# Optimization experiments

Measured on AMD Instinct MI355X. Metric: run time of the kernel, lower is better.

## Reference

```python
import jax, jax.numpy as jnp
import numpy as np
import math

D_EMBED = 1024
N_HEADS = 16
HEAD_DIM = D_EMBED // N_HEADS
ROPE_BASE = 10000.0


def apply_rope(x):
    # x: [B, S, H, D] ; torchtune-style interleaved RoPE
    B, S, H, D = x.shape
    half = D // 2
    inv_freq = 1.0 / (ROPE_BASE ** (jnp.arange(0, D, 2, dtype=jnp.float32) / D))  # [half]
    angles = jnp.arange(S, dtype=jnp.float32)[:, None] * inv_freq[None, :]        # [S, half]
    cos = jnp.cos(angles)[None, :, None, :].astype(x.dtype)  # [1,S,1,half]
    sin = jnp.sin(angles)[None, :, None, :].astype(x.dtype)
    x1 = x[..., 0::2]
    x2 = x[..., 1::2]
    o1 = x1 * cos - x2 * sin
    o2 = x1 * sin + x2 * cos
    return jnp.stack([o1, o2], axis=-1).reshape(B, S, H, D)


def setup_inputs() -> dict:
    key = jax.random.key(0)
    ks = jax.random.split(key, 7)
    B, S = 4, 2048
    d_tri = D_EMBED
    q = jax.random.normal(ks[0], (B, S, 2 * d_tri), dtype=jnp.float32)
    k = jax.random.normal(ks[1], (B, S, 2 * d_tri), dtype=jnp.float32)
    v = jax.random.normal(ks[2], (B, S, d_tri), dtype=jnp.float32)
    s_in = 1.0 / math.sqrt(2 * d_tri)
    s_tri = 1.0 / math.sqrt(d_tri)
    W_q = jax.random.normal(ks[3], (D_EMBED, 2 * d_tri), dtype=jnp.float32) * s_in
    W_k = jax.random.normal(ks[4], (D_EMBED, 2 * d_tri), dtype=jnp.float32) * s_in
    W_v = jax.random.normal(ks[5], (d_tri, d_tri), dtype=jnp.float32) * s_tri
    W_o = jax.random.normal(ks[6], (d_tri, d_tri), dtype=jnp.float32) * s_tri
    return {"q": q, "k": k, "v": v, "W_q": W_q, "W_k": W_k, "W_v": W_v, "W_o": W_o}


def reference(q, k, v, W_q, W_k, W_v, W_o):
    B, S, _ = q.shape
    H, Dh = N_HEADS, HEAD_DIM
    scale = 1.0 / math.sqrt(D_EMBED)

    qp = (q @ W_q.T).reshape(B, S, H, Dh)
    kp = (k @ W_k.T).reshape(B, S, H, Dh)
    vp = (v @ W_v.T).reshape(B, S, H, Dh)

    qp = apply_rope(qp)
    kp = apply_rope(kp)

    # [B,H,S,S]
    scores = jnp.einsum('bqhd,bkhd->bhqk', qp, kp) * scale
    causal = jnp.tril(jnp.ones((S, S), dtype=bool))
    scores = jnp.where(causal[None, None], scores, -jnp.inf)
    probs = jax.nn.softmax(scores, axis=-1)
    # dropout layers are identity in eval mode
    out = jnp.einsum('bhqk,bkhd->bqhd', probs, vp).reshape(B, S, D_EMBED)
    return out @ W_o.T
```

## Files before the change

kernel.cpp:

```cpp
#include <hip/hip_runtime.h>
#include <math.h>

#define S_LEN 2048
#define DEMB  1024
#define DH    64

typedef short bf16x8 __attribute__((ext_vector_type(8)));
typedef short bf16x4 __attribute__((ext_vector_type(4)));
typedef float floatx4 __attribute__((ext_vector_type(4)));

__device__ __forceinline__ short f2bf(float f) {
    unsigned u = __builtin_bit_cast(unsigned, f);
    u += 0x7FFFu + ((u >> 16) & 1u);
    return (short)(u >> 16);
}

__global__ void rope_table_k(float2* __restrict__ tab) {
    int idx = blockIdx.x * 256 + threadIdx.x;
    int s = idx >> 5, i = idx & 31;
    double ang = (double)s * pow(10000.0, -(double)i / 32.0);
    tab[idx] = make_float2((float)cos(ang), (float)sin(ang));
}

struct CvtArgs { const float* src[7]; short* dst[7]; int n[7]; };
__global__ __launch_bounds__(256) void cvt_k(CvtArgs a) {
    int seg = blockIdx.y;
    int idx = (blockIdx.x * 256 + threadIdx.x) * 8;
    if (idx >= a.n[seg]) return;
    const float4* s = (const float4*)(a.src[seg] + idx);
    float4 v0 = s[0], v1 = s[1];
    bf16x8 r;
    r[0] = f2bf(v0.x); r[1] = f2bf(v0.y); r[2] = f2bf(v0.z); r[3] = f2bf(v0.w);
    r[4] = f2bf(v1.x); r[5] = f2bf(v1.y); r[6] = f2bf(v1.z); r[7] = f2bf(v1.w);
    *(bf16x8*)(a.dst[seg] + idx) = r;
}

__device__ __forceinline__ void gld16(const void* g, void* l) {
    __builtin_amdgcn_global_load_lds(
        (const __attribute__((address_space(1))) void*)g,
        (__attribute__((address_space(3))) void*)l, 16, 0, 0);
}

template<int EPI>
__device__ __forceinline__ void gemm_b16_body(
    const short* __restrict__ A, const short* __restrict__ B,
    void* __restrict__ Cout, const float2* __restrict__ rope_tab,
    int M, int N, int K, short* smem)
{
    short* sA = smem;
    short* sB = smem + 128 * 32;

    const int tid  = threadIdx.x;
    const int lane = tid & 63;
    const int wv   = tid >> 6;
    const int wm   = wv >> 1, wn = wv & 1;
    const int lr   = lane & 15, quad = lane >> 4;
    const int m0   = blockIdx.y * 128, n0 = blockIdx.x * 128;

    const int rowS = tid >> 2;
    const int kkS  = (tid & 3) * 8;
    const short* gA0 = A + (size_t)(m0 + rowS) * K + kkS;
    const short* gA1 = gA0 + (size_t)64 * K;
    const short* gB0 = B + (size_t)(n0 + rowS) * K + kkS;
    const short* gB1 = gB0 + (size_t)64 * K;
    short* lA0 = sA + wv * 512;
    short* lA1 = sA + 2048 + wv * 512;
    short* lB0 = sB + wv * 512;
    short* lB1 = sB + 2048 + wv * 512;

    floatx4 acc[4][4] = {};

    for (int k0 = 0; k0 < K; k0 += 32) {
        gld16(gA0 + k0, lA0);
        gld16(gA1 + k0, lA1);
        gld16(gB0 + k0, lB0);
        gld16(gB1 + k0, lB1);
        __syncthreads();
        bf16x8 af[4], bfr[4];
        #pragma unroll
        for (int t = 0; t < 4; t++)
            af[t] = *reinterpret_cast<const bf16x8*>(&sA[(wm * 64 + t * 16 + lr) * 32 + quad * 8]);
        #pragma unroll
        for (int t = 0; t < 4; t++)
            bfr[t] = *reinterpret_cast<const bf16x8*>(&sB[(wn * 64 + t * 16 + lr) * 32 + quad * 8]);
        #pragma unroll
        for (int mt = 0; mt < 4; mt++)
            #pragma unroll
            for (int nt = 0; nt < 4; nt++)
                acc[mt][nt] = __builtin_amdgcn_mfma_f32_16x16x32_bf16(af[mt], bfr[nt], acc[mt][nt], 0, 0, 0);
        __syncthreads();
    }

    if constexpr (EPI == 0) {
        short* C = (short*)Cout;
        #pragma unroll
        for (int nt = 0; nt < 4; nt++) {
            int n_g = n0 + wn * 64 + nt * 16 + lr;
            int ii  = (n_g & 63) >> 1;
            bool evenc = (n_g & 1) == 0;
            #pragma unroll
            for (int mt = 0; mt < 4; mt++) {
                #pragma unroll
                for (int r = 0; r < 4; r++) {
                    int m_g = m0 + wm * 64 + mt * 16 + quad * 4 + r;
                    float2 cs = rope_tab[(m_g & (S_LEN - 1)) * 32 + ii];
                    float v  = acc[mt][nt][r];
                    float vn = __shfl_xor(v, 1);
                    float o = evenc ? (v * cs.x - vn * cs.y) : (v * cs.x + vn * cs.y);
                    C[(size_t)m_g * N + n_g] = f2bf(o);
                }
            }
        }
    } else if constexpr (EPI == 2) {
        float* C = (float*)Cout;
        #pragma unroll
        for (int mt = 0; mt < 4; mt++)
            #pragma unroll
            for (int r = 0; r < 4; r++) {
                size_t rowoff = (size_t)(m0 + wm * 64 + mt * 16 + quad * 4 + r) * N;
                #pragma unroll
                for (int nt = 0; nt < 4; nt++)
                    C[rowoff + n0 + wn * 64 + nt * 16 + lr] = acc[mt][nt][r];
            }
    } else {
        short* sT = smem;
        __syncthreads();
        #pragma unroll
        for (int nt = 0; nt < 4; nt++) {
            int nl = wn * 64 + nt * 16 + lr;
            #pragma unroll
            for (int mt = 0; mt < 4; mt++)
                #pragma unroll
                for (int r = 0; r < 4; r++)
                    sT[nl * 136 + wm * 64 + mt * 16 + quad * 4 + r] = f2bf(acc[mt][nt][r]);
        }
        __syncthreads();
        short* C = (short*)Cout;
        int bb = m0 >> 11;
        int s_base = m0 & (S_LEN - 1);
        #pragma unroll
        for (int i = 0; i < 8; i++) {
            int col = (tid >> 4) + i * 16;
            int mc  = (tid & 15) * 8;
            bf16x8 v = *reinterpret_cast<const bf16x8*>(&sT[col * 136 + mc]);
            size_t row = (size_t)bb * DEMB + (n0 + col);
            *reinterpret_cast<bf16x8*>(&C[row * S_LEN + s_base + mc]) = v;
        }
    }
}

template<int EPI>
__global__ __launch_bounds__(256) void gemm_b16(
    const short* __restrict__ A, const short* __restrict__ B,
    void* __restrict__ Cout, const float2* __restrict__ rope_tab,
    int M, int N, int K)
{
    __shared__ __align__(16) short smem[(EPI == 1) ? (128 * 136) : (128 * 64)];
    gemm_b16_body<EPI>(A, B, Cout, rope_tab, M, N, K, smem);
}

__global__ __launch_bounds__(256) void gemm_qk(
    const short* __restrict__ Aq, const short* __restrict__ Bq, void* __restrict__ Cq,
    const short* __restrict__ Ak, const short* __restrict__ Bk, void* __restrict__ Ck,
    const float2* __restrict__ rope_tab, int M, int N, int K)
{
    __shared__ __align__(16) short smem[128 * 64];
    if (blockIdx.z == 0)
        gemm_b16_body<0>(Aq, Bq, Cq, rope_tab, M, N, K, smem);
    else
        gemm_b16_body<0>(Ak, Bk, Ck, rope_tab, M, N, K, smem);
}

__global__ __launch_bounds__(256, 3) void flash_k(
    const short* __restrict__ qp, const short* __restrict__ kp,
    const short* __restrict__ vpT, short* __restrict__ attn)
{
    __shared__ __align__(16) short sKV[2][2][4096];
    __shared__ __align__(16) short sPb[4][2048];

    const int tid = threadIdx.x;
    const int w = tid >> 6, lane = tid & 63, lr = lane & 15, quad = lane >> 4;
    const int qt = 15 - (blockIdx.x >> 6);
    const int bh = blockIdx.x & 63;
    const int b = bh >> 4, h = bh & 15;
    const int R = qt * 128 + w * 32;
    const size_t qbase = (size_t)(b * S_LEN) * DEMB + h * DH;

    const short* kbase = kp + qbase;
    const short* vbase = vpT + ((size_t)(b * DEMB) + h * DH) * S_LEN;

    const int srow = tid >> 3;
    const int sp   = tid & 7;
    const int cs   = (sp ^ (srow & 7)) * 8;
    short* dK0 = &sKV[0][0][w * 512];  short* dV0 = &sKV[0][1][w * 512];
    short* dK1 = &sKV[1][0][w * 512];  short* dV1 = &sKV[1][1][w * 512];

    bf16x8 qf[2][2];
    #pragma unroll
    for (int mt = 0; mt < 2; mt++)
        #pragma unroll
        for (int ks = 0; ks < 2; ks++)
            qf[mt][ks] = *reinterpret_cast<const bf16x8*>(
                &qp[qbase + (size_t)(R + mt * 16 + lr) * DEMB + ks * 32 + quad * 8]);

    floatx4 oacc[2][4] = {};
    float lsum[2][4] = {};
    const float CEXP = 0.045084220081510574f;
    short* pw = sPb[w];

    const int ktend = 2 * qt + 1;

    auto stage = [&](int kt, int buf) {
        const short* kg = kbase + (size_t)kt * 64 * DEMB;
        const short* vg = vbase + kt * 64;
        short* dK = buf ? dK1 : dK0;
        short* dV = buf ? dV1 : dV0;
        gld16(kg + (size_t)srow * DEMB + cs,        dK);
        gld16(kg + (size_t)(srow + 32) * DEMB + cs, dK + 2048);
        gld16(vg + (size_t)srow * S_LEN + cs,       dV);
        gld16(vg + (size_t)(srow + 32) * S_LEN + cs, dV + 2048);
    };

    stage(0, 0);
    __syncthreads();

    for (int kt = 0; kt <= ktend; kt++) {
        const int cur = kt & 1;
        if (kt < ktend) stage(kt + 1, cur ^ 1);

        if (R + 31 >= kt * 64) {
            const short* sK = sKV[cur][0];
            const short* sV = sKV[cur][1];

            bf16x8 kf[4][2], vf[4][2];
            #pragma unroll
            for (int nt = 0; nt < 4; nt++)
                #pragma unroll
                for (int ks = 0; ks < 2; ks++) {
                    int ph = (ks * 4 + quad) ^ (lr & 7);
                    kf[nt][ks] = *reinterpret_cast<const bf16x8*>(&sK[(nt * 16 + lr) * 64 + ph * 8]);
                    vf[nt][ks] = *reinterpret_cast<const bf16x8*>(&sV[(nt * 16 + lr) * 64 + ph * 8]);
                }

            floatx4 st[2][4];
            #pragma unroll
            for (int nt = 0; nt < 4; nt++)
                #pragma unroll
                for (int mt = 0; mt < 2; mt++) {
                    floatx4 z = {};
                    z = __builtin_amdgcn_mfma_f32_16x16x32_bf16(qf[mt][0], kf[nt][0], z, 0, 0, 0);
                    st[mt][nt] = __builtin_amdgcn_mfma_f32_16x16x32_bf16(qf[mt][1], kf[nt][1], z, 0, 0, 0);
                }

            const bool need_mask = (kt * 64 + 63 > R);
            #pragma unroll
            for (int mt = 0; mt < 2; mt++)
                #pragma unroll
                for (int nt = 0; nt < 4; nt++)
                    #pragma unroll
                    for (int r = 0; r < 4; r++) {
                        float t = fminf(st[mt][nt][r] * CEXP, 80.f);
                        float p = __builtin_amdgcn_exp2f(t);
                        if (need_mask) {
                            int col = kt * 64 + nt * 16 + lr;
                            int row = R + mt * 16 + quad * 4 + r;
                            p = (col > row) ? 0.f : p;
                        }
                        st[mt][nt][r] = p;
                        lsum[mt][r] += p;
                    }

            #pragma unroll
            for (int mt = 0; mt < 2; mt++)
                #pragma unroll
                for (int nt = 0; nt < 4; nt++)
                    #pragma unroll
                    for (int r = 0; r < 4; r++) {
                        int rw = mt * 16 + quad * 4 + r;
                        int chunk = (nt * 2 + (lr >> 3)) ^ (rw & 7);
                        pw[rw * 64 + chunk * 8 + (lr & 7)] = f2bf(st[mt][nt][r]);
                    }

            bf16x8 pf[2][2];
            #pragma unroll
            for (int mt = 0; mt < 2; mt++)
                #pragma unroll
                for (int ks = 0; ks < 2; ks++) {
                    int rr = mt * 16 + lr;
                    int c  = (ks * 4 + quad) ^ (rr & 7);
                    pf[mt][ks] = *reinterpret_cast<const bf16x8*>(&pw[rr * 64 + c * 8]);
                }

            #pragma unroll
            for (int d = 0; d < 4; d++)
                #pragma unroll
                for (int mt = 0; mt < 2; mt++) {
                    oacc[mt][d] = __builtin_amdgcn_mfma_f32_16x16x32_bf16(pf[mt][0], vf[d][0], oacc[mt][d], 0, 0, 0);
                    oacc[mt][d] = __builtin_amdgcn_mfma_f32_16x16x32_bf16(pf[mt][1], vf[d][1], oacc[mt][d], 0, 0, 0);
                }
        }
        __syncthreads();
    }

    #pragma unroll
    for (int mt = 0; mt < 2; mt++)
        #pragma unroll
        for (int r = 0; r < 4; r++) {
            float l = lsum[mt][r];
            l += __shfl_xor(l, 1);
            l += __shfl_xor(l, 2);
            l += __shfl_xor(l, 4);
            l += __shfl_xor(l, 8);
            float inv = 1.f / l;
            size_t rowoff = qbase + (size_t)(R + mt * 16 + quad * 4 + r) * DEMB;
            #pragma unroll
            for (int d = 0; d < 4; d++)
                attn[rowoff + d * 16 + lr] = f2bf(oacc[mt][d][r] * inv);
        }
}

__device__ __forceinline__ bf16x4 load4(const float* p) {
    const float4 v = *reinterpret_cast<const float4*>(p);
    bf16x4 r; r[0] = f2bf(v.x); r[1] = f2bf(v.y); r[2] = f2bf(v.z); r[3] = f2bf(v.w);
    return r;
}
__device__ __forceinline__ bf16x4 load4(const short* p) {
    return *reinterpret_cast<const bf16x4*>(p);
}

template<typename TA, int EPI>
__global__ __launch_bounds__(256) void gemm_nt(
    const TA* __restrict__ A, const float* __restrict__ B,
    void* __restrict__ Cout, const float2* __restrict__ rope_tab,
    int M, int N, int K)
{
    __shared__ __align__(16) short smem[(EPI == 1) ? (128 * 136) : (2 * 128 * 40)];
    short* sA = smem;
    short* sB = smem + 128 * 40;

    const int tid  = threadIdx.x;
    const int lane = tid & 63;
    const int wv   = tid >> 6;
    const int wm   = wv >> 1, wn = wv & 1;
    const int lr   = lane & 15, quad = lane >> 4;
    const int m0   = blockIdx.y * 128, n0 = blockIdx.x * 128;

    floatx4 acc[4][4] = {};

    for (int k0 = 0; k0 < K; k0 += 32) {
        #pragma unroll
        for (int i = 0; i < 4; i++) {
            int c = tid + i * 256;
            int row = c >> 3, kc = (c & 7) << 2;
            bf16x4 v = load4(&A[(size_t)(m0 + row) * K + k0 + kc]);
            *reinterpret_cast<bf16x4*>(&sA[row * 40 + kc]) = v;
        }
        #pragma unroll
        for (int i = 0; i < 4; i++) {
            int c = tid + i * 256;
            int row = c >> 3, kc = (c & 7) << 2;
            bf16x4 v = load4(&B[(size_t)(n0 + row) * K + k0 + kc]);
            *reinterpret_cast<bf16x4*>(&sB[row * 40 + kc]) = v;
        }
        __syncthreads();
        bf16x8 af[4], bfr[4];
        #pragma unroll
        for (int t = 0; t < 4; t++)
            af[t] = *reinterpret_cast<const bf16x8*>(&sA[(wm * 64 + t * 16 + lr) * 40 + quad * 8]);
        #pragma unroll
        for (int t = 0; t < 4; t++)
            bfr[t] = *reinterpret_cast<const bf16x8*>(&sB[(wn * 64 + t * 16 + lr) * 40 + quad * 8]);
        #pragma unroll
        for (int mt = 0; mt < 4; mt++)
            #pragma unroll
            for (int nt = 0; nt < 4; nt++)
                acc[mt][nt] = __builtin_amdgcn_mfma_f32_16x16x32_bf16(af[mt], bfr[nt], acc[mt][nt], 0, 0, 0);
        __syncthreads();
    }

    if constexpr (EPI == 0) {
        short* C = (short*)Cout;
        #pragma unroll
        for (int nt = 0; nt < 4; nt++) {
            int n_g = n0 + wn * 64 + nt * 16 + lr;
            int ii  = (n_g & 63) >> 1;
            bool evenc = (n_g & 1) == 0;
            #pragma unroll
            for (int mt = 0; mt < 4; mt++) {
                #pragma unroll
                for (int r = 0; r < 4; r++) {
                    int m_g = m0 + wm * 64 + mt * 16 + quad * 4 + r;
                    float2 cs = rope_tab[(m_g & (S_LEN - 1)) * 32 + ii];
                    float v  = acc[mt][nt][r];
                    float vn = __shfl_xor(v, 1);
                    float o = evenc ? (v * cs.x - vn * cs.y) : (v * cs.x + vn * cs.y);
                    C[(size_t)m_g * N + n_g] = f2bf(o);
                }
            }
        }
    } else if constexpr (EPI == 2) {
        float* C = (float*)Cout;
        #pragma unroll
        for (int mt = 0; mt < 4; mt++)
            #pragma unroll
            for (int r = 0; r < 4; r++) {
                size_t rowoff = (size_t)(m0 + wm * 64 + mt * 16 + quad * 4 + r) * N;
                #pragma unroll
                for (int nt = 0; nt < 4; nt++)
                    C[rowoff + n0 + wn * 64 + nt * 16 + lr] = acc[mt][nt][r];
            }
    } else {
        short* sT = smem;
        __syncthreads();
        #pragma unroll
        for (int nt = 0; nt < 4; nt++) {
            int nl = wn * 64 + nt * 16 + lr;
            #pragma unroll
            for (int mt = 0; mt < 4; mt++)
                #pragma unroll
                for (int r = 0; r < 4; r++)
                    sT[nl * 136 + wm * 64 + mt * 16 + quad * 4 + r] = f2bf(acc[mt][nt][r]);
        }
        __syncthreads();
        short* C = (short*)Cout;
        int bb = m0 >> 11;
        int s_base = m0 & (S_LEN - 1);
        #pragma unroll
        for (int i = 0; i < 8; i++) {
            int col = (tid >> 4) + i * 16;
            int mc  = (tid & 15) * 8;
            bf16x8 v = *reinterpret_cast<const bf16x8*>(&sT[col * 136 + mc]);
            size_t row = (size_t)bb * DEMB + (n0 + col);
            *reinterpret_cast<bf16x8*>(&C[row * S_LEN + s_base + mc]) = v;
        }
    }
}

extern "C" void kernel_launch(void* const* d_in, const int* in_sizes, int n_in,
                              void* d_out, int out_size, void* d_ws, size_t ws_size,
                              hipStream_t stream) {
    const float* q  = (const float*)d_in[0];
    const float* k  = (const float*)d_in[1];
    const float* v  = (const float*)d_in[2];
    const float* Wq = (const float*)d_in[3];
    const float* Wk = (const float*)d_in[4];
    const float* Wv = (const float*)d_in[5];
    const float* Wo = (const float*)d_in[6];
    float* out = (float*)d_out;

    char* ws = (char*)d_ws;
    const size_t MB = 1024 * 1024;
    short*  qp   = (short*)(ws);
    short*  kp   = (short*)(ws + 16 * MB);
    short*  vpT  = (short*)(ws + 32 * MB);
    short*  attn = (short*)(ws + 48 * MB);
    float2* tab  = (float2*)(ws + 64 * MB);

    rope_table_k<<<256, 256, 0, stream>>>(tab);

    dim3 g2(8, 64);
    if (ws_size >= 157 * MB) {
        short* qb  = (short*)(ws + 65 * MB);
        short* kb  = (short*)(ws + 97 * MB);
        short* vb  = (short*)(ws + 129 * MB);
        short* wqb = (short*)(ws + 145 * MB);
        short* wkb = (short*)(ws + 149 * MB);
        short* wvb = (short*)(ws + 153 * MB);
        short* wob = (short*)(ws + 155 * MB);

        CvtArgs ca;
        ca.src[0] = q;  ca.dst[0] = qb;  ca.n[0] = 16777216;
        ca.src[1] = k;  ca.dst[1] = kb;  ca.n[1] = 16777216;
        ca.src[2] = v;  ca.dst[2] = vb;  ca.n[2] = 8388608;
        ca.src[3] = Wq; ca.dst[3] = wqb; ca.n[3] = 2097152;
        ca.src[4] = Wk; ca.dst[4] = wkb; ca.n[4] = 2097152;
        ca.src[5] = Wv; ca.dst[5] = wvb; ca.n[5] = 1048576;
        ca.src[6] = Wo; ca.dst[6] = wob; ca.n[6] = 1048576;
        cvt_k<<<dim3(8192, 7), 256, 0, stream>>>(ca);

        gemm_qk<<<dim3(8, 64, 2), 256, 0, stream>>>(qb, wqb, qp, kb, wkb, kp, tab, 8192, 1024, 2048);
        gemm_b16<1><<<g2, 256, 0, stream>>>(vb, wvb, vpT, nullptr, 8192, 1024, 1024);
        flash_k<<<1024, 256, 0, stream>>>(qp, kp, vpT, attn);
        gemm_b16<2><<<g2, 256, 0, stream>>>(attn, wob, out, nullptr, 8192, 1024, 1024);
    } else {
        gemm_nt<float, 0><<<g2, 256, 0, stream>>>(q, Wq, qp,  tab,     8192, 1024, 2048);
        gemm_nt<float, 0><<<g2, 256, 0, stream>>>(k, Wk, kp,  tab,     8192, 1024, 2048);
        gemm_nt<float, 1><<<g2, 256, 0, stream>>>(v, Wv, vpT, nullptr, 8192, 1024, 1024);
        flash_k<<<1024, 256, 0, stream>>>(qp, kp, vpT, attn);
        gemm_nt<short, 2><<<g2, 256, 0, stream>>>(attn, Wo, out, nullptr, 8192, 1024, 1024);
    }
}
```

Before: 442.6 us.

## Widen GEMM K-tile to 64 with swizzled LDS and merge QKV projections

```diff
diff --git a/kernel.cpp b/kernel.cpp
--- a/kernel.cpp
+++ b/kernel.cpp
@@ -42,13 +42,13 @@
 }
 
 template<int EPI>
-__device__ __forceinline__ void gemm_b16_body(
+__device__ __forceinline__ void gemm_body(
     const short* __restrict__ A, const short* __restrict__ B,
     void* __restrict__ Cout, const float2* __restrict__ rope_tab,
-    int M, int N, int K, short* smem)
+    int K, short* smem)
 {
     short* sA = smem;
-    short* sB = smem + 128 * 32;
+    short* sB = smem + 8192;
 
     const int tid  = threadIdx.x;
     const int lane = tid & 63;
@@ -56,60 +56,77 @@
     const int wm   = wv >> 1, wn = wv & 1;
     const int lr   = lane & 15, quad = lane >> 4;
     const int m0   = blockIdx.y * 128, n0 = blockIdx.x * 128;
-
-    const int rowS = tid >> 2;
-    const int kkS  = (tid & 3) * 8;
-    const short* gA0 = A + (size_t)(m0 + rowS) * K + kkS;
-    const short* gA1 = gA0 + (size_t)64 * K;
-    const short* gB0 = B + (size_t)(n0 + rowS) * K + kkS;
-    const short* gB1 = gB0 + (size_t)64 * K;
-    short* lA0 = sA + wv * 512;
-    short* lA1 = sA + 2048 + wv * 512;
-    short* lB0 = sB + wv * 512;
-    short* lB1 = sB + 2048 + wv * 512;
+    const int N    = 1024;
+
+    const short* gA[4]; const short* gB[4];
+    #pragma unroll
+    for (int j = 0; j < 4; j++) {
+        int c = j * 256 + tid;
+        int row = c >> 3, sp = c & 7;
+        int cs = (sp ^ (row & 7)) * 8;
+        gA[j] = A + (size_t)(m0 + row) * K + cs;
+        gB[j] = B + (size_t)(n0 + row) * K + cs;
+    }
 
     floatx4 acc[4][4] = {};
 
-    for (int k0 = 0; k0 < K; k0 += 32) {
-        gld16(gA0 + k0, lA0);
-        gld16(gA1 + k0, lA1);
-        gld16(gB0 + k0, lB0);
-        gld16(gB1 + k0, lB1);
-        __syncthreads();
-        bf16x8 af[4], bfr[4];
+    for (int k0 = 0; k0 < K; k0 += 64) {
+        #pragma unroll
+        for (int j = 0; j < 4; j++) {
+            gld16(gA[j] + k0, sA + j * 2048 + wv * 512);
+            gld16(gB[j] + k0, sB + j * 2048 + wv * 512);
+        }
+        __syncthreads();
+        bf16x8 af[4][2], bfr[4][2];
         #pragma unroll
         for (int t = 0; t < 4; t++)
-            af[t] = *reinterpret_cast<const bf16x8*>(&sA[(wm * 64 + t * 16 + lr) * 32 + quad * 8]);
-        #pragma unroll
-        for (int t = 0; t < 4; t++)
-            bfr[t] = *reinterpret_cast<const bf16x8*>(&sB[(wn * 64 + t * 16 + lr) * 32 + quad * 8]);
-        #pragma unroll
-        for (int mt = 0; mt < 4; mt++)
-            #pragma unroll
-            for (int nt = 0; nt < 4; nt++)
-                acc[mt][nt] = __builtin_amdgcn_mfma_f32_16x16x32_bf16(af[mt], bfr[nt], acc[mt][nt], 0, 0, 0);
+            #pragma unroll
+            for (int ks = 0; ks < 2; ks++) {
+                int ph = (ks * 4 + quad) ^ (lr & 7);
+                af[t][ks]  = *reinterpret_cast<const bf16x8*>(&sA[(wm * 64 + t * 16 + lr) * 64 + ph * 8]);
+                bfr[t][ks] = *reinterpret_cast<const bf16x8*>(&sB[(wn * 64 + t * 16 + lr) * 64 + ph * 8]);
+            }
+        #pragma unroll
+        for (int ks = 0; ks < 2; ks++)
+            #pragma unroll
+            for (int mt = 0; mt < 4; mt++)
+                #pragma unroll
+                for (int nt = 0; nt < 4; nt++)
+                    acc[mt][nt] = __builtin_amdgcn_mfma_f32_16x16x32_bf16(af[mt][ks], bfr[nt][ks], acc[mt][nt], 0, 0, 0);
         __syncthreads();
     }
 
     if constexpr (EPI == 0) {
-        short* C = (short*)Cout;
+        unsigned* sTi = (unsigned*)smem;
         #pragma unroll
         for (int nt = 0; nt < 4; nt++) {
-            int n_g = n0 + wn * 64 + nt * 16 + lr;
-            int ii  = (n_g & 63) >> 1;
-            bool evenc = (n_g & 1) == 0;
-            #pragma unroll
-            for (int mt = 0; mt < 4; mt++) {
+            int n_l = wn * 64 + nt * 16 + lr;
+            int ii  = ((n0 + n_l) & 63) >> 1;
+            #pragma unroll
+            for (int mt = 0; mt < 4; mt++)
                 #pragma unroll
                 for (int r = 0; r < 4; r++) {
-                    int m_g = m0 + wm * 64 + mt * 16 + quad * 4 + r;
-                    float2 cs = rope_tab[(m_g & (S_LEN - 1)) * 32 + ii];
+                    int row_l = wm * 64 + mt * 16 + quad * 4 + r;
+                    float2 cs = rope_tab[((m0 + row_l) & (S_LEN - 1)) * 32 + ii];
                     float v  = acc[mt][nt][r];
                     float vn = __shfl_xor(v, 1);
-                    float o = evenc ? (v * cs.x - vn * cs.y) : (v * cs.x + vn * cs.y);
-                    C[(size_t)m_g * N + n_g] = f2bf(o);
+                    float o0 = v * cs.x - vn * cs.y;
+                    float o1 = vn * cs.x + v * cs.y;
+                    if (!(lr & 1)) {
+                        unsigned pk = (unsigned)(unsigned short)f2bf(o0) |
+                                      ((unsigned)(unsigned short)f2bf(o1) << 16);
+                        sTi[row_l * 68 + (n_l >> 1)] = pk;
+                    }
                 }
-            }
+        }
+        __syncthreads();
+        short* C = (short*)Cout;
+        #pragma unroll
+        for (int j = 0; j < 8; j++) {
+            int c = j * 256 + tid;
+            int row = c >> 4, col = (c & 15) * 8;
+            bf16x8 val = *reinterpret_cast<const bf16x8*>(&smem[row * 136 + col]);
+            *reinterpret_cast<bf16x8*>(&C[(size_t)(m0 + row) * N + n0 + col]) = val;
         }
     } else if constexpr (EPI == 2) {
         float* C = (float*)Cout;
@@ -124,7 +141,6 @@
             }
     } else {
         short* sT = smem;
-        __syncthreads();
         #pragma unroll
         for (int nt = 0; nt < 4; nt++) {
             int nl = wn * 64 + nt * 16 + lr;
@@ -149,26 +165,26 @@
     }
 }
 
-template<int EPI>
-__global__ __launch_bounds__(256) void gemm_b16(
-    const short* __restrict__ A, const short* __restrict__ B,
-    void* __restrict__ Cout, const float2* __restrict__ rope_tab,
-    int M, int N, int K)
-{
-    __shared__ __align__(16) short smem[(EPI == 1) ? (128 * 136) : (128 * 64)];
-    gemm_b16_body<EPI>(A, B, Cout, rope_tab, M, N, K, smem);
-}
-
-__global__ __launch_bounds__(256) void gemm_qk(
+__global__ __launch_bounds__(256, 3) void gemm_proj(
     const short* __restrict__ Aq, const short* __restrict__ Bq, void* __restrict__ Cq,
     const short* __restrict__ Ak, const short* __restrict__ Bk, void* __restrict__ Ck,
-    const float2* __restrict__ rope_tab, int M, int N, int K)
+    const short* __restrict__ Av, const short* __restrict__ Bv, void* __restrict__ Cv,
+    const float2* __restrict__ rope_tab)
 {
-    __shared__ __align__(16) short smem[128 * 64];
+    __shared__ __align__(16) short smem[17408];
     if (blockIdx.z == 0)
-        gemm_b16_body<0>(Aq, Bq, Cq, rope_tab, M, N, K, smem);
+        gemm_body<0>(Aq, Bq, Cq, rope_tab, 2048, smem);
+    else if (blockIdx.z == 1)
+        gemm_body<0>(Ak, Bk, Ck, rope_tab, 2048, smem);
     else
-        gemm_b16_body<0>(Ak, Bk, Ck, rope_tab, M, N, K, smem);
+        gemm_body<1>(Av, Bv, Cv, nullptr, 1024, smem);
+}
+
+__global__ __launch_bounds__(256, 3) void gemm_out(
+    const short* __restrict__ A, const short* __restrict__ B, void* __restrict__ Cout)
+{
+    __shared__ __align__(16) short smem[17408];
+    gemm_body<2>(A, B, Cout, nullptr, 1024, smem);
 }
 
 __global__ __launch_bounds__(256, 3) void flash_k(
@@ -478,10 +494,10 @@
         ca.src[6] = Wo; ca.dst[6] = wob; ca.n[6] = 1048576;
         cvt_k<<<dim3(8192, 7), 256, 0, stream>>>(ca);
 
-        gemm_qk<<<dim3(8, 64, 2), 256, 0, stream>>>(qb, wqb, qp, kb, wkb, kp, tab, 8192, 1024, 2048);
-        gemm_b16<1><<<g2, 256, 0, stream>>>(vb, wvb, vpT, nullptr, 8192, 1024, 1024);
+        gemm_proj<<<dim3(8, 64, 3), 256, 0, stream>>>(
+            qb, wqb, qp, kb, wkb, kp, vb, wvb, vpT, tab);
         flash_k<<<1024, 256, 0, stream>>>(qp, kp, vpT, attn);
-        gemm_b16<2><<<g2, 256, 0, stream>>>(attn, wob, out, nullptr, 8192, 1024, 1024);
+        gemm_out<<<g2, 256, 0, stream>>>(attn, wob, out);
     } else {
         gemm_nt<float, 0><<<g2, 256, 0, stream>>>(q, Wq, qp,  tab,     8192, 1024, 2048);
         gemm_nt<float, 0><<<g2, 256, 0, stream>>>(k, Wk, kp,  tab,     8192, 1024, 2048);
```

After: 419.9 us. -5.1%, faster.
